# Optimization experiments

Measured on AMD Instinct MI355X. Metric: run time of the kernel, lower is better.

The kernel has to match this reference:

```python
import jax, jax.numpy as jnp
import numpy as np

D = 2048      # hidden_size
H = 16        # num_heads
DH = D // H   # head_dim
DFF = 8192    # intermediate_size
EPS = 1e-6


def setup_inputs() -> dict:
    key = jax.random.key(0)
    ks = jax.random.split(key, 12)
    s = 0.02
    return {
        "x": jax.random.normal(ks[0], (2, 2048, D), dtype=jnp.float32),
        "wq": jax.random.normal(ks[1], (D, D), dtype=jnp.float32) * s,
        "bq": jnp.zeros((D,), dtype=jnp.float32),
        "wk": jax.random.normal(ks[2], (D, D), dtype=jnp.float32) * s,
        "bk": jnp.zeros((D,), dtype=jnp.float32),
        "wv": jax.random.normal(ks[3], (D, D), dtype=jnp.float32) * s,
        "bv": jnp.zeros((D,), dtype=jnp.float32),
        "wo": jax.random.normal(ks[4], (D, D), dtype=jnp.float32) * s,
        "bo": jnp.zeros((D,), dtype=jnp.float32),
        "w_gate": jax.random.normal(ks[5], (DFF, D), dtype=jnp.float32) * s,
        "w_up": jax.random.normal(ks[6], (DFF, D), dtype=jnp.float32) * s,
        "w_down": jax.random.normal(ks[7], (D, DFF), dtype=jnp.float32) * s,
        "g_att": jnp.ones((D,), dtype=jnp.float32),
        "g_ffn": jnp.ones((D,), dtype=jnp.float32),
    }


def _rmsnorm(x, w):
    # Faithful to source: multiplies by sqrt(mean(x^2)+eps) (source bug kept).
    var = jnp.mean(x * x, axis=-1, keepdims=True)
    return x * jnp.sqrt(var + EPS) * w


def _mha(x, wq, bq, wk, bk, wv, bv, wo, bo):
    B, S, _ = x.shape
    def split(t):  # [B,S,D] -> [B,H,S,DH]
        return t.reshape(B, S, H, DH).transpose(0, 2, 1, 3)
    q = split(x @ wq.T + bq)
    k = split(x @ wk.T + bk)
    v = split(x @ wv.T + bv)
    scores = jnp.einsum("bhsd,bhtd->bhst", q, k) / jnp.sqrt(jnp.float32(DH))
    probs = jax.nn.softmax(scores, axis=-1)
    out = jnp.einsum("bhst,bhtd->bhsd", probs, v)       # [B,H,S,DH]
    # Faithful quirk: transpose(-1,-2) (NOT (1,2)), then view(B,-1,D)
    out = out.transpose(0, 1, 3, 2).reshape(B, S, D)    # scrambled layout, as in source
    return out @ wo.T + bo


def _ffn(x, w_gate, w_up, w_down):
    inter = jax.nn.relu(x @ w_gate.T) * (x @ w_up.T)
    return inter @ w_down.T


def reference(x, wq, bq, wk, bk, wv, bv, wo, bo, w_gate, w_up, w_down, g_att, g_ffn):
    h = x + _mha(_rmsnorm(x, g_att), wq, bq, wk, bk, wv, bv, wo, bo)
    out = h + _ffn(_rmsnorm(h, g_ffn), w_gate, w_up, w_down)
    return out
```

## Files before the change

### kernel.cpp

```cpp
#include <hip/hip_runtime.h>

typedef __attribute__((ext_vector_type(8))) short short8;
typedef __attribute__((ext_vector_type(4))) float f32x4;
typedef __attribute__((ext_vector_type(4))) unsigned short us4;
typedef unsigned short u16;

__device__ __forceinline__ u16 f2bf(float f) {
    unsigned u = __builtin_bit_cast(unsigned, f);
    return (u16)((u + 0x7fffu + ((u >> 16) & 1u)) >> 16);
}
__device__ __forceinline__ float bf2f(u16 h) {
    unsigned u = ((unsigned)h) << 16;
    return __builtin_bit_cast(float, u);
}
__device__ __forceinline__ void async16(const void* g, void* l) {
    __builtin_amdgcn_global_load_lds((const __attribute__((address_space(1))) unsigned int*)g,
                                     (__attribute__((address_space(3))) unsigned int*)l,
                                     16, 0, 0);
}

__global__ __launch_bounds__(256) void cvt_k(const float* __restrict__ in, u16* __restrict__ out) {
    int i = (blockIdx.x * 256 + threadIdx.x) * 4;
    f32x4 v = *(const f32x4*)(in + i);
    us4 o;
    o[0] = f2bf(v[0]); o[1] = f2bf(v[1]); o[2] = f2bf(v[2]); o[3] = f2bf(v[3]);
    *(us4*)(out + i) = o;
}

__global__ __launch_bounds__(256) void rmsnorm_k(const float* __restrict__ X, const float* __restrict__ g,
                                                 u16* __restrict__ O) {
    const int row = blockIdx.x, tid = threadIdx.x;
    const float* xr = X + (long)row * 2048 + tid * 8;
    f32x4 v0 = *(const f32x4*)xr;
    f32x4 v1 = *(const f32x4*)(xr + 4);
    float ss = v0[0]*v0[0] + v0[1]*v0[1] + v0[2]*v0[2] + v0[3]*v0[3]
             + v1[0]*v1[0] + v1[1]*v1[1] + v1[2]*v1[2] + v1[3]*v1[3];
#pragma unroll
    for (int m = 1; m < 64; m <<= 1) ss += __shfl_xor(ss, m, 64);
    __shared__ float wsum[4];
    if ((tid & 63) == 0) wsum[tid >> 6] = ss;
    __syncthreads();
    float tot = wsum[0] + wsum[1] + wsum[2] + wsum[3];
    const float sc = sqrtf(tot * (1.0f / 2048.0f) + 1e-6f);
    const float* gr = g + tid * 8;
    f32x4 g0 = *(const f32x4*)gr, g1 = *(const f32x4*)(gr + 4);
    us4 o0, o1;
    o0[0] = f2bf(v0[0] * sc * g0[0]); o0[1] = f2bf(v0[1] * sc * g0[1]);
    o0[2] = f2bf(v0[2] * sc * g0[2]); o0[3] = f2bf(v0[3] * sc * g0[3]);
    o1[0] = f2bf(v1[0] * sc * g1[0]); o1[1] = f2bf(v1[1] * sc * g1[1]);
    o1[2] = f2bf(v1[2] * sc * g1[2]); o1[3] = f2bf(v1[3] * sc * g1[3]);
    u16* op = O + (long)row * 2048 + tid * 8;
    *(us4*)op = o0;
    *(us4*)(op + 4) = o1;
}

enum { M_QKV = 0, M_VT = 1, M_H1 = 2, M_RELU = 3, M_MUL = 4, M_ADD = 5 };

template <int MODE>
__global__ __launch_bounds__(256) void gemm_bt(const u16* __restrict__ A, const u16* __restrict__ W,
                                               const float* __restrict__ bias, const float* resid,
                                               const u16* aux, void* out,
                                               int N, int K, float scale) {
    __shared__ u16 As[128 * 32];
    __shared__ u16 Bs[128 * 32];
    const int tid = threadIdx.x, wv = tid >> 6, lane = tid & 63;
    const int q4 = lane >> 4, lr = lane & 15;
    const long m0 = (long)blockIdx.y * 128;
    const int n0 = blockIdx.x * 128;
    const int wm = (wv >> 1) * 64, wn = (wv & 1) * 64;
    f32x4 acc[4][4] = {};

    const int r0 = tid >> 2, b0 = (tid & 3) * 8;
    const int r1 = 64 + r0;
    u16* lA0 = As + (wv * 64) * 8;
    u16* lA1 = As + (256 + wv * 64) * 8;
    u16* lB0 = Bs + (wv * 64) * 8;
    u16* lB1 = Bs + (256 + wv * 64) * 8;
    const u16* a0 = A + (m0 + r0) * (long)K + b0;
    const u16* a1 = A + (m0 + r1) * (long)K + b0;
    const u16* w0 = W + (long)(n0 + r0) * K + b0;
    const u16* w1 = W + (long)(n0 + r1) * K + b0;

    for (int k0 = 0; k0 < K; k0 += 32) {
        __syncthreads();
        async16(a0 + k0, lA0);
        async16(a1 + k0, lA1);
        async16(w0 + k0, lB0);
        async16(w1 + k0, lB1);
        __syncthreads();
        short8 af[4], bf[4];
#pragma unroll
        for (int i = 0; i < 4; i++) af[i] = *(const short8*)(As + (wm + i * 16 + lr) * 32 + q4 * 8);
#pragma unroll
        for (int j = 0; j < 4; j++) bf[j] = *(const short8*)(Bs + (wn + j * 16 + lr) * 32 + q4 * 8);
#pragma unroll
        for (int i = 0; i < 4; i++)
#pragma unroll
            for (int j = 0; j < 4; j++)
                acc[i][j] = __builtin_amdgcn_mfma_f32_16x16x32_bf16(af[i], bf[j], acc[i][j], 0, 0, 0);
    }

#pragma unroll
    for (int i = 0; i < 4; i++) {
#pragma unroll
        for (int j = 0; j < 4; j++) {
            const int gn = n0 + wn + j * 16 + lr;
#pragma unroll
            for (int r = 0; r < 4; r++) {
                const long gm = m0 + wm + i * 16 + q4 * 4 + r;
                float v = acc[i][j][r];
                if constexpr (MODE == M_QKV) {
                    v = (v + bias[gn]) * scale;
                    ((u16*)out)[gm * N + gn] = f2bf(v);
                } else if constexpr (MODE == M_VT) {
                    v = v + bias[gm];
                    const long b = gn >> 11, s = gn & 2047;
                    ((u16*)out)[(b << 22) + gm * 2048 + s] = f2bf(v);
                } else if constexpr (MODE == M_H1) {
                    ((float*)out)[gm * N + gn] = v + bias[gn] + resid[gm * N + gn];
                } else if constexpr (MODE == M_RELU) {
                    ((u16*)out)[gm * N + gn] = f2bf(fmaxf(v, 0.0f));
                } else if constexpr (MODE == M_MUL) {
                    ((u16*)out)[gm * N + gn] = f2bf(v * bf2f(aux[gm * N + gn]));
                } else {
                    ((float*)out)[gm * N + gn] = v + resid[gm * N + gn];
                }
            }
        }
    }
}

__global__ __launch_bounds__(512) void attn_kernel(const u16* __restrict__ Q, const u16* __restrict__ Km,
                                                   const u16* __restrict__ Vt, u16* __restrict__ Oscr) {
    __shared__ u16 Ks[128 * 128];
    __shared__ u16 Vs[128 * 128];
    __shared__ u16 Ps[8][16 * 136];
    __shared__ float abuf[8][16];
    __shared__ float lbuf[8][16];
    const int tid = threadIdx.x, w = tid >> 6, lane = tid & 63;
    const int q4 = lane >> 4, lr = lane & 15;
    const int bh = blockIdx.y, b = bh >> 4, h = bh & 15;
    const int sw = blockIdx.x * 128 + w * 16;
    const long qkbase = ((long)b * 2048) * 2048 + h * 128;
    const long vtbase = ((long)b * 2048 + h * 128) * 2048;

    short8 qf[4];
    {
        const u16* qr = Q + qkbase + (long)(sw + lr) * 2048 + q4 * 8;
#pragma unroll
        for (int kk = 0; kk < 4; kk++) qf[kk] = *(const short8*)(qr + kk * 32);
    }
    float m_i[4], l_i[4];
#pragma unroll
    for (int r = 0; r < 4; r++) { m_i[r] = -1e30f; l_i[r] = 0.0f; }
    f32x4 oacc[8] = {};

    for (int t0 = 0; t0 < 2048; t0 += 128) {
        __syncthreads();
#pragma unroll
        for (int i = 0; i < 4; i++) {
            const int c = i * 512 + tid;
            const int row = c >> 4;
            const int lc = (c & 15) ^ (row & 15);
            async16(Km + qkbase + (long)(t0 + row) * 2048 + lc * 8, (u16*)Ks + (i * 512 + w * 64) * 8);
            async16(Vt + vtbase + (long)row * 2048 + t0 + lc * 8, (u16*)Vs + (i * 512 + w * 64) * 8);
        }
        __syncthreads();
        f32x4 sacc[8] = {};
#pragma unroll
        for (int kk = 0; kk < 4; kk++) {
#pragma unroll
            for (int n = 0; n < 8; n++) {
                const int pc = (kk * 4 + q4) ^ lr;
                short8 kf = *(const short8*)(Ks + ((n * 16 + lr) * 16 + pc) * 8);
                sacc[n] = __builtin_amdgcn_mfma_f32_16x16x32_bf16(qf[kk], kf, sacc[n], 0, 0, 0);
            }
        }
        float al[4];
#pragma unroll
        for (int r = 0; r < 4; r++) {
            float mx = sacc[0][r];
#pragma unroll
            for (int n = 1; n < 8; n++) mx = fmaxf(mx, sacc[n][r]);
#pragma unroll
            for (int msk = 1; msk < 16; msk <<= 1) mx = fmaxf(mx, __shfl_xor(mx, msk, 64));
            const float mn = fmaxf(m_i[r], mx);
            al[r] = __expf(m_i[r] - mn);
            float rs = 0.0f;
#pragma unroll
            for (int n = 0; n < 8; n++) {
                float p = __expf(sacc[n][r] - mn);
                sacc[n][r] = p;
                rs += p;
            }
#pragma unroll
            for (int msk = 1; msk < 16; msk <<= 1) rs += __shfl_xor(rs, msk, 64);
            l_i[r] = l_i[r] * al[r] + rs;
            m_i[r] = mn;
        }
#pragma unroll
        for (int n = 0; n < 8; n++)
#pragma unroll
            for (int r = 0; r < 4; r++)
                Ps[w][(q4 * 4 + r) * 136 + n * 16 + lr] = f2bf(sacc[n][r]);
        if (lr == 0) {
#pragma unroll
            for (int r = 0; r < 4; r++) abuf[w][q4 * 4 + r] = al[r];
        }
        __syncthreads();
        const float a_s = abuf[w][lr];
#pragma unroll
        for (int mm = 0; mm < 8; mm++) oacc[mm] *= a_s;
#pragma unroll
        for (int kk = 0; kk < 4; kk++) {
            short8 pf = *(const short8*)(&Ps[w][lr * 136 + kk * 32 + q4 * 8]);
            const int pc = (kk * 4 + q4) ^ lr;
#pragma unroll
            for (int mm = 0; mm < 8; mm++) {
                short8 vf = *(const short8*)(Vs + ((mm * 16 + lr) * 16 + pc) * 8);
                oacc[mm] = __builtin_amdgcn_mfma_f32_16x16x32_bf16(vf, pf, oacc[mm], 0, 0, 0);
            }
        }
    }
    if (lr == 0) {
#pragma unroll
        for (int r = 0; r < 4; r++) lbuf[w][q4 * 4 + r] = l_i[r];
    }
    __syncthreads();
    const float linv = 1.0f / lbuf[w][lr];
#pragma unroll
    for (int mm = 0; mm < 8; mm++) {
#pragma unroll
        for (int r = 0; r < 4; r++) {
            const int d = mm * 16 + q4 * 4 + r;
            Oscr[vtbase + (long)d * 2048 + sw + lr] = f2bf(oacc[mm][r] * linv);
        }
    }
}

extern "C" void kernel_launch(void* const* d_in, const int* in_sizes, int n_in,
                              void* d_out, int out_size, void* d_ws, size_t ws_size,
                              hipStream_t stream) {
    const float* x  = (const float*)d_in[0];
    const float* wq = (const float*)d_in[1];
    const float* bq = (const float*)d_in[2];
    const float* wk = (const float*)d_in[3];
    const float* bk = (const float*)d_in[4];
    const float* wv = (const float*)d_in[5];
    const float* bv = (const float*)d_in[6];
    const float* wo = (const float*)d_in[7];
    const float* bo = (const float*)d_in[8];
    const float* wg = (const float*)d_in[9];
    const float* wu = (const float*)d_in[10];
    const float* wd = (const float*)d_in[11];
    const float* ga = (const float*)d_in[12];
    const float* gf = (const float*)d_in[13];

    char* ws = (char*)d_ws;
    const size_t MB = (size_t)1 << 20;
    u16*  xn    = (u16*)(ws + 0);
    u16*  scr   = (u16*)(ws + 0);
    u16*  hn    = (u16*)(ws + 0);
    u16*  qb    = (u16*)(ws + 16 * MB);
    u16*  kb    = (u16*)(ws + 32 * MB);
    u16*  vt    = (u16*)(ws + 48 * MB);
    u16*  grelu = (u16*)(ws + 16 * MB);
    u16*  inter = grelu;
    u16*  wreg  = (u16*)(ws + 80 * MB);
    u16*  wq_b  = wreg;
    u16*  wk_b  = wreg + 4 * MB;
    u16*  wv_b  = wreg + 8 * MB;
    u16*  wo_b  = wreg + 12 * MB;
    u16*  wbig  = wreg;
    float* h1   = (float*)d_out;

    cvt_k<<<4096, 256, 0, stream>>>(wq, wq_b);
    cvt_k<<<4096, 256, 0, stream>>>(wk, wk_b);
    cvt_k<<<4096, 256, 0, stream>>>(wv, wv_b);
    cvt_k<<<4096, 256, 0, stream>>>(wo, wo_b);

    rmsnorm_k<<<4096, 256, 0, stream>>>(x, ga, xn);

    const float qscale = 0.08838834764831843f;
    gemm_bt<M_QKV><<<dim3(16, 32), 256, 0, stream>>>(xn, wq_b, bq, nullptr, nullptr, qb, 2048, 2048, qscale);
    gemm_bt<M_QKV><<<dim3(16, 32), 256, 0, stream>>>(xn, wk_b, bk, nullptr, nullptr, kb, 2048, 2048, 1.0f);
    gemm_bt<M_VT><<<dim3(32, 16), 256, 0, stream>>>(wv_b, xn, bv, nullptr, nullptr, vt, 4096, 2048, 1.0f);

    attn_kernel<<<dim3(16, 32), 512, 0, stream>>>(qb, kb, vt, scr);

    gemm_bt<M_H1><<<dim3(16, 32), 256, 0, stream>>>(scr, wo_b, bo, x, nullptr, h1, 2048, 2048, 1.0f);

    cvt_k<<<16384, 256, 0, stream>>>(wg, wbig);
    rmsnorm_k<<<4096, 256, 0, stream>>>(h1, gf, hn);

    gemm_bt<M_RELU><<<dim3(64, 32), 256, 0, stream>>>(hn, wbig, nullptr, nullptr, nullptr, grelu, 8192, 2048, 1.0f);

    cvt_k<<<16384, 256, 0, stream>>>(wu, wbig);
    gemm_bt<M_MUL><<<dim3(64, 32), 256, 0, stream>>>(hn, wbig, nullptr, nullptr, grelu, inter, 8192, 2048, 1.0f);

    cvt_k<<<16384, 256, 0, stream>>>(wd, wbig);
    gemm_bt<M_ADD><<<dim3(16, 32), 256, 0, stream>>>(inter, wbig, nullptr, h1, nullptr, d_out, 2048, 8192, 1.0f);
}
```

Baseline: 1.249 ms.

## Replace GEMM with 8-wave multi-buffered pipelined kernel with swizzled LDS and XCD remap

Replaces the simple single-buffered 128x128 GEMM with a 512-thread kernel using 256-row tiles (BN 128 or 256), a four-deep LDS ring of async global-to-LDS loads interleaved with MFMA phases, XOR-swizzled LDS columns to avoid bank conflicts, and a workgroup remap that spreads tiles across the 8 XCDs. It targets the exposed load latency and the barrier stalls of the old loop, where each K step waited for its loads before computing. In exchange it uses more LDS and registers per block, relies on hand-placed vmcnt waits that must match the issue order exactly, and assumes K is a multiple of 128 and M, N divide the tile sizes.

New measurement: 1.126 ms. 9.8% less time.

```diff
diff --git a/kernel.cpp b/kernel.cpp
--- a/kernel.cpp
+++ b/kernel.cpp
@@ -56,59 +56,120 @@
 
 enum { M_QKV = 0, M_VT = 1, M_H1 = 2, M_RELU = 3, M_MUL = 4, M_ADD = 5 };
 
-template <int MODE>
-__global__ __launch_bounds__(256) void gemm_bt(const u16* __restrict__ A, const u16* __restrict__ W,
-                                               const float* __restrict__ bias, const float* resid,
-                                               const u16* aux, void* out,
-                                               int N, int K, float scale) {
-    __shared__ u16 As[128 * 32];
-    __shared__ u16 Bs[128 * 32];
+template <int MODE, int BN>
+__global__ __launch_bounds__(512, 2) void gemm8p(const u16* __restrict__ A, const u16* __restrict__ W,
+                                                 const float* __restrict__ bias, const float* resid,
+                                                 const u16* aux, void* out,
+                                                 int N, int K, float scale) {
+    constexpr int MF = BN / 32;
+    constexpr int HF = MF / 2;
+    constexpr int NF = 4;
+    constexpr int BSLOT = BN * 32;
+    __shared__ alignas(16) u16 As[2][2][8192];
+    __shared__ alignas(16) u16 Bs[2][2][BSLOT];
+
     const int tid = threadIdx.x, wv = tid >> 6, lane = tid & 63;
     const int q4 = lane >> 4, lr = lane & 15;
-    const long m0 = (long)blockIdx.y * 128;
-    const int n0 = blockIdx.x * 128;
-    const int wm = (wv >> 1) * 64, wn = (wv & 1) * 64;
-    f32x4 acc[4][4] = {};
-
-    const int r0 = tid >> 2, b0 = (tid & 3) * 8;
-    const int r1 = 64 + r0;
-    u16* lA0 = As + (wv * 64) * 8;
-    u16* lA1 = As + (256 + wv * 64) * 8;
-    u16* lB0 = Bs + (wv * 64) * 8;
-    u16* lB1 = Bs + (256 + wv * 64) * 8;
-    const u16* a0 = A + (m0 + r0) * (long)K + b0;
-    const u16* a1 = A + (m0 + r1) * (long)K + b0;
-    const u16* w0 = W + (long)(n0 + r0) * K + b0;
-    const u16* w1 = W + (long)(n0 + r1) * K + b0;
-
-    for (int k0 = 0; k0 < K; k0 += 32) {
-        __syncthreads();
-        async16(a0 + k0, lA0);
-        async16(a1 + k0, lA1);
-        async16(w0 + k0, lB0);
-        async16(w1 + k0, lB1);
-        __syncthreads();
-        short8 af[4], bf[4];
-#pragma unroll
-        for (int i = 0; i < 4; i++) af[i] = *(const short8*)(As + (wm + i * 16 + lr) * 32 + q4 * 8);
-#pragma unroll
-        for (int j = 0; j < 4; j++) bf[j] = *(const short8*)(Bs + (wn + j * 16 + lr) * 32 + q4 * 8);
-#pragma unroll
-        for (int i = 0; i < 4; i++)
-#pragma unroll
-            for (int j = 0; j < 4; j++)
-                acc[i][j] = __builtin_amdgcn_mfma_f32_16x16x32_bf16(af[i], bf[j], acc[i][j], 0, 0, 0);
-    }
-
-#pragma unroll
-    for (int i = 0; i < 4; i++) {
-#pragma unroll
-        for (int j = 0; j < 4; j++) {
-            const int gn = n0 + wn + j * 16 + lr;
+    const int wm = (BN == 256) ? (wv >> 2) * 128 : (wv >> 1) * 64;
+    const int wn = (BN == 256) ? (wv & 3) * 64 : (wv & 1) * 64;
+
+    const int ntn = N / BN;
+    int wg = blockIdx.x;
+    {
+        const int nwg = gridDim.x, q = nwg >> 3, r = nwg & 7, x = wg & 7, l = wg >> 3;
+        wg = (x < r ? x * (q + 1) : r * (q + 1) + (x - r) * q) + l;
+    }
+    const long m0 = (long)(wg / ntn) * 256;
+    const int n0 = (wg % ntn) * BN;
+
+    const int cswz = (q4 ^ ((lr >> 1) & 3)) * 8;
+    const int a_rd = (wm + lr) * 32 + cswz;
+    const int b_rd = (wn + lr) * 32 + cswz;
+
+    const int srow = tid >> 2;
+    const int slc = ((tid & 3) ^ ((srow >> 1) & 3)) * 8;
+    const u16* gA0 = A + (m0 + srow) * (long)K + slc;
+    const u16* gA1 = gA0 + 128 * (long)K;
+    const u16* gB0 = W + ((long)n0 + srow) * K + slc;
+    const u16* gB1 = (BN == 256) ? gB0 + 128 * (long)K : gB0;
+
+    f32x4 acc[MF][NF] = {};
+    short8 bfr[NF];
+
+#define STAGEA(BUF, KS, KOFF) do {                       \
+        u16* d_ = &As[BUF][KS][wv * 512];                \
+        async16(gA0 + (KOFF), d_);                       \
+        async16(gA1 + (KOFF), d_ + 4096); } while (0)
+#define STAGEB(BUF, KS, KOFF) do {                       \
+        u16* d_ = &Bs[BUF][KS][wv * 512];                \
+        async16(gB0 + (KOFF), d_);                       \
+        if (BN == 256) async16(gB1 + (KOFF), d_ + 4096); } while (0)
+#define VMW_N do { if (BN == 256) asm volatile("s_waitcnt vmcnt(6)" ::: "memory"); \
+                   else           asm volatile("s_waitcnt vmcnt(4)" ::: "memory"); } while (0)
+#define VMW_0 asm volatile("s_waitcnt vmcnt(0)" ::: "memory")
+#define PHASE(BUF, KS, FSEL, STAGE_, VMW_) do {                                              \
+        short8 afr_[HF];                                                                     \
+        _Pragma("unroll") for (int m_ = 0; m_ < HF; m_++)                                    \
+            afr_[m_] = *(const short8*)(&As[BUF][KS][a_rd + ((FSEL) * HF + m_) * 512]);      \
+        if ((FSEL) == 0) {                                                                   \
+            _Pragma("unroll") for (int n_ = 0; n_ < NF; n_++)                                \
+                bfr[n_] = *(const short8*)(&Bs[BUF][KS][b_rd + n_ * 512]);                   \
+        }                                                                                    \
+        STAGE_;                                                                              \
+        __builtin_amdgcn_s_barrier();                                                        \
+        asm volatile("s_waitcnt lgkmcnt(0)");                                                \
+        __builtin_amdgcn_s_setprio(1);                                                       \
+        _Pragma("unroll") for (int m_ = 0; m_ < HF; m_++)                                    \
+            _Pragma("unroll") for (int n_ = 0; n_ < NF; n_++)                                \
+                acc[(FSEL) * HF + m_][n_] = __builtin_amdgcn_mfma_f32_16x16x32_bf16(         \
+                    afr_[m_], bfr[n_], acc[(FSEL) * HF + m_][n_], 0, 0, 0);                  \
+        __builtin_amdgcn_s_setprio(0);                                                       \
+        VMW_;                                                                                \
+        __builtin_amdgcn_sched_barrier(0);                                                   \
+        __builtin_amdgcn_s_barrier();                                                        \
+    } while (0)
+
+    STAGEB(0, 0, 0);  STAGEA(0, 0, 0);  STAGEB(0, 1, 32); STAGEA(0, 1, 32);
+    STAGEB(1, 0, 64); STAGEA(1, 0, 64); STAGEB(1, 1, 96);
+    VMW_N;
+    __builtin_amdgcn_s_barrier();
+
+    const int NI = K >> 7;
+    int k0 = 0;
+    for (int i = 0; i < NI - 1; ++i, k0 += 128) {
+        PHASE(0, 0, 0, STAGEA(1, 1, k0 + 96),  );
+        PHASE(0, 0, 1, STAGEB(0, 0, k0 + 128), );
+        PHASE(0, 1, 0, STAGEA(0, 0, k0 + 128), );
+        PHASE(0, 1, 1, STAGEB(0, 1, k0 + 160), VMW_N);
+        PHASE(1, 0, 0, STAGEA(0, 1, k0 + 160), );
+        PHASE(1, 0, 1, STAGEB(1, 0, k0 + 192), );
+        PHASE(1, 1, 0, STAGEA(1, 0, k0 + 192), );
+        PHASE(1, 1, 1, STAGEB(1, 1, k0 + 224), VMW_N);
+    }
+    PHASE(0, 0, 0, STAGEA(1, 1, k0 + 96), );
+    PHASE(0, 0, 1, , );
+    PHASE(0, 1, 0, , );
+    PHASE(0, 1, 1, , VMW_0);
+    PHASE(1, 0, 0, , );
+    PHASE(1, 0, 1, , );
+    PHASE(1, 1, 0, , );
+    PHASE(1, 1, 1, , );
+
+#undef PHASE
+#undef VMW_0
+#undef VMW_N
+#undef STAGEB
+#undef STAGEA
+
+#pragma unroll
+    for (int m = 0; m < MF; m++) {
+#pragma unroll
+        for (int n = 0; n < NF; n++) {
+            const int gn = n0 + wn + n * 16 + lr;
 #pragma unroll
             for (int r = 0; r < 4; r++) {
-                const long gm = m0 + wm + i * 16 + q4 * 4 + r;
-                float v = acc[i][j][r];
+                const long gm = m0 + wm + m * 16 + q4 * 4 + r;
+                float v = acc[m][n][r];
                 if constexpr (MODE == M_QKV) {
                     v = (v + bias[gn]) * scale;
                     ((u16*)out)[gm * N + gn] = f2bf(v);
@@ -282,22 +343,22 @@
     rmsnorm_k<<<4096, 256, 0, stream>>>(x, ga, xn);
 
     const float qscale = 0.08838834764831843f;
-    gemm_bt<M_QKV><<<dim3(16, 32), 256, 0, stream>>>(xn, wq_b, bq, nullptr, nullptr, qb, 2048, 2048, qscale);
-    gemm_bt<M_QKV><<<dim3(16, 32), 256, 0, stream>>>(xn, wk_b, bk, nullptr, nullptr, kb, 2048, 2048, 1.0f);
-    gemm_bt<M_VT><<<dim3(32, 16), 256, 0, stream>>>(wv_b, xn, bv, nullptr, nullptr, vt, 4096, 2048, 1.0f);
+    gemm8p<M_QKV, 128><<<256, 512, 0, stream>>>(xn, wq_b, bq, nullptr, nullptr, qb, 2048, 2048, qscale);
+    gemm8p<M_QKV, 128><<<256, 512, 0, stream>>>(xn, wk_b, bk, nullptr, nullptr, kb, 2048, 2048, 1.0f);
+    gemm8p<M_VT, 128><<<256, 512, 0, stream>>>(wv_b, xn, bv, nullptr, nullptr, vt, 4096, 2048, 1.0f);
 
     attn_kernel<<<dim3(16, 32), 512, 0, stream>>>(qb, kb, vt, scr);
 
-    gemm_bt<M_H1><<<dim3(16, 32), 256, 0, stream>>>(scr, wo_b, bo, x, nullptr, h1, 2048, 2048, 1.0f);
+    gemm8p<M_H1, 128><<<256, 512, 0, stream>>>(scr, wo_b, bo, x, nullptr, h1, 2048, 2048, 1.0f);
 
     cvt_k<<<16384, 256, 0, stream>>>(wg, wbig);
     rmsnorm_k<<<4096, 256, 0, stream>>>(h1, gf, hn);
 
-    gemm_bt<M_RELU><<<dim3(64, 32), 256, 0, stream>>>(hn, wbig, nullptr, nullptr, nullptr, grelu, 8192, 2048, 1.0f);
+    gemm8p<M_RELU, 256><<<512, 512, 0, stream>>>(hn, wbig, nullptr, nullptr, nullptr, grelu, 8192, 2048, 1.0f);
 
     cvt_k<<<16384, 256, 0, stream>>>(wu, wbig);
-    gemm_bt<M_MUL><<<dim3(64, 32), 256, 0, stream>>>(hn, wbig, nullptr, nullptr, grelu, inter, 8192, 2048, 1.0f);
+    gemm8p<M_MUL, 256><<<512, 512, 0, stream>>>(hn, wbig, nullptr, nullptr, grelu, inter, 8192, 2048, 1.0f);
 
     cvt_k<<<16384, 256, 0, stream>>>(wd, wbig);
-    gemm_bt<M_ADD><<<dim3(16, 32), 256, 0, stream>>>(inter, wbig, nullptr, h1, nullptr, d_out, 2048, 8192, 1.0f);
-}
+    gemm8p<M_ADD, 128><<<256, 512, 0, stream>>>(inter, wbig, nullptr, h1, nullptr, d_out, 2048, 8192, 1.0f);
+}
```

## Rewrite GEMM with 4-stage async LDS pipeline, swizzled LDS, XCD-aware block remap

Applied to the files above, without the earlier changes.

Replaces the single-buffered GEMM, which synchronized twice per 32-wide K step, with a four-slot ring of LDS buffers. Global-to-LDS async loads are issued three stages ahead, paced with vmcnt waits, and the MFMA blocks are raised in priority. LDS columns are XOR-swizzled to avoid bank conflicts, and a 1D grid is remapped so consecutive tiles land on the same XCD for L2 locality. The changes add LDS use (64KB per block) and code complexity, and assume K is a multiple of 128.

Result: faster. 1.123 ms (-10.1%).

```diff
diff --git a/kernel.cpp b/kernel.cpp
--- a/kernel.cpp
+++ b/kernel.cpp
@@ -57,58 +57,98 @@
 enum { M_QKV = 0, M_VT = 1, M_H1 = 2, M_RELU = 3, M_MUL = 4, M_ADD = 5 };
 
 template <int MODE>
-__global__ __launch_bounds__(256) void gemm_bt(const u16* __restrict__ A, const u16* __restrict__ W,
-                                               const float* __restrict__ bias, const float* resid,
-                                               const u16* aux, void* out,
-                                               int N, int K, float scale) {
-    __shared__ u16 As[128 * 32];
-    __shared__ u16 Bs[128 * 32];
+__global__ __launch_bounds__(256, 2) void gemm4p(const u16* __restrict__ A, const u16* __restrict__ W,
+                                                 const float* __restrict__ bias, const float* resid,
+                                                 const u16* aux, void* out,
+                                                 int N, int K, float scale) {
+    __shared__ alignas(16) u16 As[2][2][4096];
+    __shared__ alignas(16) u16 Bs[2][2][4096];
+
     const int tid = threadIdx.x, wv = tid >> 6, lane = tid & 63;
     const int q4 = lane >> 4, lr = lane & 15;
-    const long m0 = (long)blockIdx.y * 128;
-    const int n0 = blockIdx.x * 128;
     const int wm = (wv >> 1) * 64, wn = (wv & 1) * 64;
+
+    const int ntn = N >> 7;
+    int wg = blockIdx.x;
+    {
+        const int nwg = gridDim.x, q = nwg >> 3, r = nwg & 7, x = wg & 7, l = wg >> 3;
+        wg = (x < r ? x * (q + 1) : r * (q + 1) + (x - r) * q) + l;
+    }
+    const long m0 = (long)(wg / ntn) * 128;
+    const int n0 = (wg % ntn) * 128;
+
+    const int cswz = (q4 ^ ((lr >> 1) & 3)) * 8;
+    const int a_rd = (wm + lr) * 32 + cswz;
+    const int b_rd = (wn + lr) * 32 + cswz;
+
+    const int srow = tid >> 2;
+    const int slc = ((tid & 3) ^ ((srow >> 1) & 3)) * 8;
+    const u16* gA0 = A + (m0 + srow) * (long)K + slc;
+    const u16* gA1 = gA0 + 64 * (long)K;
+    const u16* gB0 = W + ((long)n0 + srow) * K + slc;
+    const u16* gB1 = gB0 + 64 * (long)K;
+
     f32x4 acc[4][4] = {};
 
-    const int r0 = tid >> 2, b0 = (tid & 3) * 8;
-    const int r1 = 64 + r0;
-    u16* lA0 = As + (wv * 64) * 8;
-    u16* lA1 = As + (256 + wv * 64) * 8;
-    u16* lB0 = Bs + (wv * 64) * 8;
-    u16* lB1 = Bs + (256 + wv * 64) * 8;
-    const u16* a0 = A + (m0 + r0) * (long)K + b0;
-    const u16* a1 = A + (m0 + r1) * (long)K + b0;
-    const u16* w0 = W + (long)(n0 + r0) * K + b0;
-    const u16* w1 = W + (long)(n0 + r1) * K + b0;
-
-    for (int k0 = 0; k0 < K; k0 += 32) {
-        __syncthreads();
-        async16(a0 + k0, lA0);
-        async16(a1 + k0, lA1);
-        async16(w0 + k0, lB0);
-        async16(w1 + k0, lB1);
-        __syncthreads();
-        short8 af[4], bf[4];
-#pragma unroll
-        for (int i = 0; i < 4; i++) af[i] = *(const short8*)(As + (wm + i * 16 + lr) * 32 + q4 * 8);
-#pragma unroll
-        for (int j = 0; j < 4; j++) bf[j] = *(const short8*)(Bs + (wn + j * 16 + lr) * 32 + q4 * 8);
-#pragma unroll
-        for (int i = 0; i < 4; i++)
-#pragma unroll
-            for (int j = 0; j < 4; j++)
-                acc[i][j] = __builtin_amdgcn_mfma_f32_16x16x32_bf16(af[i], bf[j], acc[i][j], 0, 0, 0);
-    }
-
-#pragma unroll
-    for (int i = 0; i < 4; i++) {
-#pragma unroll
-        for (int j = 0; j < 4; j++) {
-            const int gn = n0 + wn + j * 16 + lr;
+#define STAGE(BUF, KS, KOFF) do {                        \
+        u16* dA_ = &As[BUF][KS][wv * 512];               \
+        async16(gA0 + (KOFF), dA_);                      \
+        async16(gA1 + (KOFF), dA_ + 2048);               \
+        u16* dB_ = &Bs[BUF][KS][wv * 512];               \
+        async16(gB0 + (KOFF), dB_);                      \
+        async16(gB1 + (KOFF), dB_ + 2048); } while (0)
+#define VM(N) asm volatile("s_waitcnt vmcnt(" #N ")")
+#define BAR __builtin_amdgcn_s_barrier()
+#define PHASE(BUF, KS, STAGE_, VMW_) do {                                                    \
+        short8 af_[4], bf_[4];                                                               \
+        _Pragma("unroll") for (int m_ = 0; m_ < 4; m_++)                                     \
+            af_[m_] = *(const short8*)(&As[BUF][KS][a_rd + m_ * 512]);                       \
+        _Pragma("unroll") for (int n_ = 0; n_ < 4; n_++)                                     \
+            bf_[n_] = *(const short8*)(&Bs[BUF][KS][b_rd + n_ * 512]);                       \
+        STAGE_;                                                                              \
+        BAR;                                                                                 \
+        asm volatile("s_waitcnt lgkmcnt(0)");                                                \
+        __builtin_amdgcn_s_setprio(1);                                                       \
+        _Pragma("unroll") for (int m_ = 0; m_ < 4; m_++)                                     \
+            _Pragma("unroll") for (int n_ = 0; n_ < 4; n_++)                                 \
+                acc[m_][n_] = __builtin_amdgcn_mfma_f32_16x16x32_bf16(                       \
+                    af_[m_], bf_[n_], acc[m_][n_], 0, 0, 0);                                 \
+        __builtin_amdgcn_s_setprio(0);                                                       \
+        VMW_;                                                                                \
+        BAR;                                                                                 \
+    } while (0)
+
+    const int NI = K >> 7;
+    int k0 = 0;
+
+    STAGE(0, 0, 0); STAGE(0, 1, 32); STAGE(1, 0, 64);
+    VM(8);
+    BAR;
+    for (int i = 0; i < NI - 1; ++i, k0 += 128) {
+        PHASE(0, 0, STAGE(1, 1, k0 + 96),  VM(4));
+        PHASE(0, 1, STAGE(0, 0, k0 + 128), VM(4));
+        PHASE(1, 0, STAGE(0, 1, k0 + 160), VM(4));
+        PHASE(1, 1, STAGE(1, 0, k0 + 192), VM(4));
+    }
+    PHASE(0, 0, STAGE(1, 1, k0 + 96), VM(4));
+    PHASE(0, 1, , VM(4));
+    PHASE(1, 0, , VM(0));
+    PHASE(1, 1, , );
+
+#undef PHASE
+#undef BAR
+#undef VM
+#undef STAGE
+
+#pragma unroll
+    for (int m = 0; m < 4; m++) {
+#pragma unroll
+        for (int n = 0; n < 4; n++) {
+            const int gn = n0 + wn + n * 16 + lr;
 #pragma unroll
             for (int r = 0; r < 4; r++) {
-                const long gm = m0 + wm + i * 16 + q4 * 4 + r;
-                float v = acc[i][j][r];
+                const long gm = m0 + wm + m * 16 + q4 * 4 + r;
+                float v = acc[m][n][r];
                 if constexpr (MODE == M_QKV) {
                     v = (v + bias[gn]) * scale;
                     ((u16*)out)[gm * N + gn] = f2bf(v);
@@ -282,22 +322,22 @@
     rmsnorm_k<<<4096, 256, 0, stream>>>(x, ga, xn);
 
     const float qscale = 0.08838834764831843f;
-    gemm_bt<M_QKV><<<dim3(16, 32), 256, 0, stream>>>(xn, wq_b, bq, nullptr, nullptr, qb, 2048, 2048, qscale);
-    gemm_bt<M_QKV><<<dim3(16, 32), 256, 0, stream>>>(xn, wk_b, bk, nullptr, nullptr, kb, 2048, 2048, 1.0f);
-    gemm_bt<M_VT><<<dim3(32, 16), 256, 0, stream>>>(wv_b, xn, bv, nullptr, nullptr, vt, 4096, 2048, 1.0f);
+    gemm4p<M_QKV><<<512, 256, 0, stream>>>(xn, wq_b, bq, nullptr, nullptr, qb, 2048, 2048, qscale);
+    gemm4p<M_QKV><<<512, 256, 0, stream>>>(xn, wk_b, bk, nullptr, nullptr, kb, 2048, 2048, 1.0f);
+    gemm4p<M_VT><<<512, 256, 0, stream>>>(wv_b, xn, bv, nullptr, nullptr, vt, 4096, 2048, 1.0f);
 
     attn_kernel<<<dim3(16, 32), 512, 0, stream>>>(qb, kb, vt, scr);
 
-    gemm_bt<M_H1><<<dim3(16, 32), 256, 0, stream>>>(scr, wo_b, bo, x, nullptr, h1, 2048, 2048, 1.0f);
+    gemm4p<M_H1><<<512, 256, 0, stream>>>(scr, wo_b, bo, x, nullptr, h1, 2048, 2048, 1.0f);
 
     cvt_k<<<16384, 256, 0, stream>>>(wg, wbig);
     rmsnorm_k<<<4096, 256, 0, stream>>>(h1, gf, hn);
 
-    gemm_bt<M_RELU><<<dim3(64, 32), 256, 0, stream>>>(hn, wbig, nullptr, nullptr, nullptr, grelu, 8192, 2048, 1.0f);
+    gemm4p<M_RELU><<<2048, 256, 0, stream>>>(hn, wbig, nullptr, nullptr, nullptr, grelu, 8192, 2048, 1.0f);
 
     cvt_k<<<16384, 256, 0, stream>>>(wu, wbig);
-    gemm_bt<M_MUL><<<dim3(64, 32), 256, 0, stream>>>(hn, wbig, nullptr, nullptr, grelu, inter, 8192, 2048, 1.0f);
+    gemm4p<M_MUL><<<2048, 256, 0, stream>>>(hn, wbig, nullptr, nullptr, grelu, inter, 8192, 2048, 1.0f);
 
     cvt_k<<<16384, 256, 0, stream>>>(wd, wbig);
-    gemm_bt<M_ADD><<<dim3(16, 32), 256, 0, stream>>>(inter, wbig, nullptr, h1, nullptr, d_out, 2048, 8192, 1.0f);
-}
+    gemm4p<M_ADD><<<512, 256, 0, stream>>>(inter, wbig, nullptr, h1, nullptr, d_out, 2048, 8192, 1.0f);
+}
```
